# Kernel optimization log

Hardware: AMD Instinct MI355X
Metric: run time of the kernel (lower is better)

## Reference

```python
import jax, jax.numpy as jnp
import numpy as np

EPS = 1e-5

def _binarize(x):
    # torch.sign with 0 -> +1 (module maps sign==0 to 1)
    return jnp.where(x >= 0, 1.0, -1.0).astype(x.dtype)

def _conv(x, w, stride):
    return jax.lax.conv_general_dilated(
        x, w, window_strides=(stride, stride), padding=((1, 1), (1, 1)),
        dimension_numbers=('NCHW', 'OIHW', 'NCHW'))

def _bn(x, g, b, m, v):
    # eval-mode BatchNorm2d with running stats
    inv = g / jnp.sqrt(v + EPS)
    return x * inv[None, :, None, None] + (b - m * inv)[None, :, None, None]

def setup_inputs() -> dict:
    key = jax.random.key(0)
    ks = jax.random.split(key, 16)
    d = {
        'x': jax.random.normal(ks[0], (32, 3, 224, 224), jnp.float32),
        'conv1_w': jax.random.normal(ks[1], (32, 3, 3, 3), jnp.float32),
        'conv2_w': jax.random.normal(ks[2], (64, 32, 3, 3), jnp.float32),
        'conv3_w': jax.random.normal(ks[3], (128, 64, 3, 3), jnp.float32),
        'bn1_g': jax.random.normal(ks[4], (32,), jnp.float32),
        'bn1_b': jax.random.normal(ks[5], (32,), jnp.float32),
        'bn1_m': jax.random.normal(ks[6], (32,), jnp.float32),
        'bn1_v': jax.random.uniform(ks[7], (32,), jnp.float32, 0.5, 1.5),
        'bn2_g': jax.random.normal(ks[8], (64,), jnp.float32),
        'bn2_b': jax.random.normal(ks[9], (64,), jnp.float32),
        'bn2_m': jax.random.normal(ks[10], (64,), jnp.float32),
        'bn2_v': jax.random.uniform(ks[11], (64,), jnp.float32, 0.5, 1.5),
        'bn3_g': jax.random.normal(ks[12], (128,), jnp.float32),
        'bn3_b': jax.random.normal(ks[13], (128,), jnp.float32),
        'bn3_m': jax.random.normal(ks[14], (128,), jnp.float32),
        'bn3_v': jax.random.uniform(ks[15], (128,), jnp.float32, 0.5, 1.5),
        'fc_w': jax.random.normal(jax.random.fold_in(key, 99), (2, 128), jnp.float32) * 0.1,
        'fc_b': jnp.zeros((2,), jnp.float32),
    }
    return d

def reference(x, conv1_w, conv2_w, conv3_w,
              bn1_g, bn1_b, bn1_m, bn1_v,
              bn2_g, bn2_b, bn2_m, bn2_v,
              bn3_g, bn3_b, bn3_m, bn3_v,
              fc_w, fc_b):
    # layer 1: binarized conv -> BN -> sign
    h = _binarize(_bn(_conv(_binarize(x), _binarize(conv1_w), 1), bn1_g, bn1_b, bn1_m, bn1_v))  # [B,32,224,224]
    # layer 2 (stride 2)
    h = _binarize(_bn(_conv(_binarize(h), _binarize(conv2_w), 2), bn2_g, bn2_b, bn2_m, bn2_v))  # [B,64,112,112]
    # layer 3 (stride 2)
    h = _binarize(_bn(_conv(_binarize(h), _binarize(conv3_w), 2), bn3_g, bn3_b, bn3_m, bn3_v))  # [B,128,56,56]
    # adaptive avg pool to 1x1 + fc
    h = jnp.mean(h, axis=(2, 3))  # [B,128]
    return h @ fc_w.T + fc_b      # [B,2]
```

## Files before the change

### kernel.cpp

```cpp
#include <hip/hip_runtime.h>
#include <cstdint>
#include <cstddef>


__device__ __align__(16) uint32_t g_h1p[32 * 224 * 224];
__device__ __align__(16) uint32_t g_h2lo[32 * 112 * 112];
__device__ __align__(16) uint32_t g_h2hi[32 * 112 * 112];
__device__ uint32_t g_w1p[32];
__device__ uint32_t g_w2p[576];
__device__ uint64_t g_w3p[1152];
__device__ float    g_inv1[32],  g_sh1[32];
__device__ float    g_inv2[64],  g_sh2[64];
__device__ float    g_inv3[128], g_sh3[128];
__device__ int      g_thr1[32];
__device__ uint32_t g_pol1;
__device__ int      g_thr2[64];
__device__ uint32_t g_pol2[2];
__device__ int      g_acc[32 * 128];

__device__ __forceinline__ int bn_neg(int s, float inv, float sh) {
    float y = __fadd_rn(__fmul_rn((float)s, inv), sh);
    return (y < 0.0f) ? 1 : 0;
}

__global__ void prep_kernel(
    const float* __restrict__ w1, const float* __restrict__ w2, const float* __restrict__ w3,
    const float* __restrict__ g1, const float* __restrict__ b1, const float* __restrict__ m1, const float* __restrict__ v1,
    const float* __restrict__ g2, const float* __restrict__ b2, const float* __restrict__ m2, const float* __restrict__ v2,
    const float* __restrict__ g3, const float* __restrict__ b3, const float* __restrict__ m3, const float* __restrict__ v3)
{
    int tid = blockIdx.x * blockDim.x + threadIdx.x;
    int lt  = threadIdx.x;

    if (tid < 32 * 128) g_acc[tid] = 0;

    if (tid < 32) {
        uint32_t m = 0;
        for (int t = 0; t < 27; ++t)
            m |= (w1[tid * 27 + t] < 0.0f ? 1u : 0u) << t;
        g_w1p[tid] = m;
    }
    if (tid < 576) {
        int oc = tid / 9, tap = tid % 9, ky = tap / 3, kx = tap % 3;
        uint32_t m = 0;
        for (int ic = 0; ic < 32; ++ic)
            m |= (w2[((oc * 32 + ic) * 3 + ky) * 3 + kx] < 0.0f ? 1u : 0u) << ic;
        g_w2p[tid] = m;
    }
    if (tid < 1152) {
        int oc = tid / 9, tap = tid % 9, ky = tap / 3, kx = tap % 3;
        uint64_t m = 0;
        for (int ic = 0; ic < 64; ++ic)
            m |= (uint64_t)(w3[((oc * 64 + ic) * 3 + ky) * 3 + kx] < 0.0f ? 1u : 0u) << ic;
        g_w3p[tid] = m;
    }

    if (blockIdx.x == 0) {
        if (lt < 32) {
            float inv = __fdiv_rn(g1[lt], __fsqrt_rn(__fadd_rn(v1[lt], 1e-5f)));
            g_inv1[lt] = inv;
            g_sh1[lt] = __fsub_rn(b1[lt], __fmul_rn(m1[lt], inv));
        } else if (lt < 96) {
            int c = lt - 32;
            float inv = __fdiv_rn(g2[c], __fsqrt_rn(__fadd_rn(v2[c], 1e-5f)));
            g_inv2[c] = inv;
            g_sh2[c] = __fsub_rn(b2[c], __fmul_rn(m2[c], inv));
        } else if (lt < 224) {
            int c = lt - 96;
            float inv = __fdiv_rn(g3[c], __fsqrt_rn(__fadd_rn(v3[c], 1e-5f)));
            g_inv3[c] = inv;
            g_sh3[c] = __fsub_rn(b3[c], __fmul_rn(m3[c], inv));
        }
        __syncthreads();

        __shared__ uint32_t p1bits[32];
        __shared__ uint32_t p2bits[64];
        if (lt < 32) {
            float inv = g_inv1[lt], sh = g_sh1[lt];
            int P = bn_neg(27 - 2 * 27, inv, sh);
            int M = 28;
            for (int m = 0; m <= 27; ++m)
                if (bn_neg(27 - 2 * m, inv, sh) == P) { M = m; break; }
            g_thr1[lt] = M;
            p1bits[lt] = (uint32_t)P;
        }
        if (lt >= 64 && lt < 128) {
            int c = lt - 64;
            float inv = g_inv2[c], sh = g_sh2[c];
            int P = bn_neg(288 - 2 * 288, inv, sh);
            int M = 289;
            for (int m = 0; m <= 288; ++m)
                if (bn_neg(288 - 2 * m, inv, sh) == P) { M = m; break; }
            g_thr2[c] = M;
            p2bits[c] = (uint32_t)P;
        }
        __syncthreads();
        if (lt == 0) {
            uint32_t p = 0;
            for (int i = 0; i < 32; ++i) p |= p1bits[i] << i;
            g_pol1 = p;
            uint32_t plo = 0, phi = 0;
            for (int i = 0; i < 32; ++i) { plo |= p2bits[i] << i; phi |= p2bits[32 + i] << i; }
            g_pol2[0] = plo; g_pol2[1] = phi;
        }
    }
}

__global__ void layer1_kernel(const float* __restrict__ x)
{
    int idx = blockIdx.x * blockDim.x + threadIdx.x;
    const int total = 32 * 224 * 56;
    if (idx >= total) return;
    int xq = idx % 56;
    int t  = idx / 56;
    int yy = t % 224;
    int b  = t / 224;
    int xx0 = xq * 4;

    const float* xb = x + (size_t)b * 3 * 224 * 224;
    uint32_t outw[4];

    bool interior = (yy >= 1) && (yy <= 222) && (xq >= 1) && (xq <= 54);
    if (interior) {
        uint32_t cb[3][3];
#pragma unroll
        for (int ic = 0; ic < 3; ++ic)
#pragma unroll
        for (int r = 0; r < 3; ++r) {
            const float* p = xb + ((size_t)ic * 224 + (yy - 1 + r)) * 224 + (xx0 - 1);
            uint32_t bits = 0;
#pragma unroll
            for (int j = 0; j < 6; ++j)
                bits |= (p[j] < 0.0f ? 1u : 0u) << j;
            cb[ic][r] = bits;
        }
        uint32_t xm[4];
#pragma unroll
        for (int p = 0; p < 4; ++p) {
            uint32_t m = 0;
#pragma unroll
            for (int ic = 0; ic < 3; ++ic)
#pragma unroll
            for (int r = 0; r < 3; ++r)
                m |= ((cb[ic][r] >> p) & 7u) << (ic * 9 + r * 3);
            xm[p] = m;
        }
#pragma unroll
        for (int p = 0; p < 4; ++p) outw[p] = 0;
#pragma unroll
        for (int oc = 0; oc < 32; ++oc) {
            uint32_t w = g_w1p[oc];
            int M = g_thr1[oc];
#pragma unroll
            for (int p = 0; p < 4; ++p) {
                int mm = __popc(xm[p] ^ w);
                outw[p] |= (mm < M ? 1u : 0u) << oc;
            }
        }
        uint32_t pol = g_pol1;
#pragma unroll
        for (int p = 0; p < 4; ++p) outw[p] ^= pol;
    } else {
#pragma unroll
        for (int p = 0; p < 4; ++p) {
            int xx = xx0 + p;
            uint32_t xmask = 0, vmask = 0;
#pragma unroll
            for (int ky = 0; ky < 3; ++ky) {
                int iy = yy - 1 + ky;
                bool vy = (iy >= 0 && iy < 224);
#pragma unroll
                for (int kx = 0; kx < 3; ++kx) {
                    int ix = xx - 1 + kx;
                    bool v = vy && (ix >= 0) && (ix < 224);
                    if (v) {
                        int sp = ky * 3 + kx;
#pragma unroll
                        for (int ic = 0; ic < 3; ++ic) {
                            float val = xb[((size_t)ic * 224 + iy) * 224 + ix];
                            xmask |= (val < 0.0f ? 1u : 0u) << (ic * 9 + sp);
                            vmask |= 1u << (ic * 9 + sp);
                        }
                    }
                }
            }
            int nvalid = __popc(vmask);
            uint32_t ow = 0;
#pragma unroll
            for (int oc = 0; oc < 32; ++oc) {
                int mism = __popc((xmask ^ g_w1p[oc]) & vmask);
                int s = nvalid - 2 * mism;
                float y = __fadd_rn(__fmul_rn((float)s, g_inv1[oc]), g_sh1[oc]);
                ow |= (y < 0.0f ? 1u : 0u) << oc;
            }
            outw[p] = ow;
        }
    }
    uint4 o = make_uint4(outw[0], outw[1], outw[2], outw[3]);
    *(uint4*)&g_h1p[((size_t)b * 224 + yy) * 224 + xx0] = o;
}

__global__ void layer2_kernel()
{
    int half = blockIdx.y;
    int idx = blockIdx.x * blockDim.x + threadIdx.x;
    const int total = 32 * 112 * 112;
    if (idx >= total) return;
    int ox = idx % 112;
    int t = idx / 112;
    int oy = t % 112;
    int b = t / 112;

    const uint32_t* hb = g_h1p + (size_t)b * 224 * 224;
    const uint32_t* wp = g_w2p + half * 288;
    uint32_t outw = 0;

    if (ox >= 1 && oy >= 1) {
        uint32_t hw[9];
#pragma unroll
        for (int ky = 0; ky < 3; ++ky) {
            const uint32_t* row = hb + (2 * oy - 1 + ky) * 224 + (2 * ox - 1);
            hw[ky * 3 + 0] = row[0];
            hw[ky * 3 + 1] = row[1];
            hw[ky * 3 + 2] = row[2];
        }
        const int* thr = g_thr2 + half * 32;
        for (int oc = 0; oc < 32; ++oc) {
            int m = 0;
#pragma unroll
            for (int tt = 0; tt < 9; ++tt)
                m += __popc(hw[tt] ^ wp[oc * 9 + tt]);
            outw |= (m < thr[oc] ? 1u : 0u) << oc;
        }
        outw ^= g_pol2[half];
    } else {
        uint32_t hw[9];
        bool tv[9];
        int nvt = 0;
#pragma unroll
        for (int ky = 0; ky < 3; ++ky) {
            int iy = 2 * oy - 1 + ky;
            bool vy = (iy >= 0 && iy < 224);
#pragma unroll
            for (int kx = 0; kx < 3; ++kx) {
                int ix = 2 * ox - 1 + kx;
                bool v = vy && (ix >= 0) && (ix < 224);
                int tt = ky * 3 + kx;
                tv[tt] = v;
                nvt += v ? 1 : 0;
                hw[tt] = v ? hb[iy * 224 + ix] : 0u;
            }
        }
        int base = 32 * nvt;
        const float* invp = g_inv2 + half * 32;
        const float* shp  = g_sh2  + half * 32;
        for (int oc = 0; oc < 32; ++oc) {
            int s = 0;
#pragma unroll
            for (int tt = 0; tt < 9; ++tt) {
                uint32_t w = wp[oc * 9 + tt];
                s += __popc(hw[tt] ^ (tv[tt] ? w : 0u));
            }
            int val = base - 2 * s;
            float y = __fadd_rn(__fmul_rn((float)val, invp[oc]), shp[oc]);
            outw |= (y < 0.0f ? 1u : 0u) << oc;
        }
    }
    if (half == 0) g_h2lo[idx] = outw; else g_h2hi[idx] = outw;
}

__global__ void layer3_kernel()
{
    int ocq = blockIdx.z;
    int b = blockIdx.y;
    int pix = blockIdx.x * blockDim.x + threadIdx.x;
    bool valid = pix < 56 * 56;
    int oy = valid ? pix / 56 : 0;
    int ox = valid ? pix % 56 : 0;

    const uint32_t* hlo = g_h2lo + (size_t)b * 112 * 112;
    const uint32_t* hhi = g_h2hi + (size_t)b * 112 * 112;
    uint64_t hw[9];
    bool tv[9];
    int nvt = 0;
#pragma unroll
    for (int ky = 0; ky < 3; ++ky) {
        int iy = 2 * oy - 1 + ky;
        bool vy = (iy >= 0 && iy < 112);
#pragma unroll
        for (int kx = 0; kx < 3; ++kx) {
            int ix = 2 * ox - 1 + kx;
            bool v = valid && vy && (ix >= 0) && (ix < 112);
            int tt = ky * 3 + kx;
            tv[tt] = v;
            nvt += v ? 1 : 0;
            hw[tt] = v ? ((uint64_t)hlo[iy * 112 + ix] | ((uint64_t)hhi[iy * 112 + ix] << 32)) : 0ull;
        }
    }
    int base = 64 * nvt;
    int lane = threadIdx.x & 63;
    unsigned long long am = __ballot(valid ? 1 : 0);
    int nact = __popcll(am);

    const uint64_t* wp = g_w3p + ocq * 288;
    const float* invp = g_inv3 + ocq * 32;
    const float* shp  = g_sh3  + ocq * 32;
    for (int oc = 0; oc < 32; ++oc) {
        int s = 0;
#pragma unroll
        for (int tt = 0; tt < 9; ++tt) {
            uint64_t w = wp[oc * 9 + tt];
            s += __popcll(hw[tt] ^ (tv[tt] ? w : 0ull));
        }
        int val = base - 2 * s;
        float y = __fadd_rn(__fmul_rn((float)val, invp[oc]), shp[oc]);
        int neg = (valid && y < 0.0f) ? 1 : 0;
        unsigned long long bm = __ballot(neg);
        if (lane == 0) {
            int cneg = __popcll(bm);
            atomicAdd(&g_acc[b * 128 + ocq * 32 + oc], nact - 2 * cneg);
        }
    }
}

__global__ void fc_kernel(
    const float* __restrict__ fc_w, const float* __restrict__ fc_b,
    float* __restrict__ out)
{
    int tid = threadIdx.x;
    if (tid >= 64) return;
    int b = tid >> 1, k = tid & 1;
    float s = fc_b[k];
    for (int oc = 0; oc < 128; ++oc) {
        float h = __fdiv_rn((float)g_acc[b * 128 + oc], 3136.0f);
        s = __fadd_rn(s, __fmul_rn(h, fc_w[k * 128 + oc]));
    }
    out[b * 2 + k] = s;
}

extern "C" void kernel_launch(void* const* d_in, const int* in_sizes, int n_in,
                              void* d_out, int out_size, void* d_ws, size_t ws_size,
                              hipStream_t stream)
{
    const float* x   = (const float*)d_in[0];
    const float* w1  = (const float*)d_in[1];
    const float* w2  = (const float*)d_in[2];
    const float* w3  = (const float*)d_in[3];
    const float* g1  = (const float*)d_in[4];
    const float* b1  = (const float*)d_in[5];
    const float* m1  = (const float*)d_in[6];
    const float* v1  = (const float*)d_in[7];
    const float* g2  = (const float*)d_in[8];
    const float* b2  = (const float*)d_in[9];
    const float* m2  = (const float*)d_in[10];
    const float* v2  = (const float*)d_in[11];
    const float* g3  = (const float*)d_in[12];
    const float* b3  = (const float*)d_in[13];
    const float* m3  = (const float*)d_in[14];
    const float* v3  = (const float*)d_in[15];
    const float* fcw = (const float*)d_in[16];
    const float* fcb = (const float*)d_in[17];
    float* out = (float*)d_out;
    (void)d_ws; (void)ws_size; (void)in_sizes; (void)n_in; (void)out_size;

    prep_kernel<<<16, 256, 0, stream>>>(w1, w2, w3,
        g1, b1, m1, v1, g2, b2, m2, v2, g3, b3, m3, v3);

    {
        int total = 32 * 224 * 56;
        layer1_kernel<<<(total + 255) / 256, 256, 0, stream>>>(x);
    }
    {
        int total = 32 * 112 * 112;
        dim3 grid((total + 255) / 256, 2);
        layer2_kernel<<<grid, 256, 0, stream>>>();
    }
    {
        dim3 grid((56 * 56 + 255) / 256, 32, 4);
        layer3_kernel<<<grid, 256, 0, stream>>>();
    }
    fc_kernel<<<1, 64, 0, stream>>>(fcw, fcb, out);
}
```

Measured before the change: 233.7 us.

## Split interior and border work into separate blocks with per-pattern padding thresholds

Layers 1 and 2 now give interior pixels and border pixels their own block ranges, so warps no longer diverge between the fast popcount path and the slow float BN path. For each border pattern the prep kernel precomputes a threshold that folds in the invalid padded taps, so border pixels can use a plain popcount compare as well. Layer 1's interior loads switch to float4 reads. In exchange the prep kernel does more serial work in block 0, including threshold searches for three tap-count classes, and the border index mapping is more involved.

```diff
diff --git a/kernel.cpp b/kernel.cpp
--- a/kernel.cpp
+++ b/kernel.cpp
@@ -12,10 +12,10 @@
 __device__ float    g_inv1[32],  g_sh1[32];
 __device__ float    g_inv2[64],  g_sh2[64];
 __device__ float    g_inv3[128], g_sh3[128];
-__device__ int      g_thr1[32];
-__device__ uint32_t g_pol1;
-__device__ int      g_thr2[64];
-__device__ uint32_t g_pol2[2];
+__device__ int      g_Mb1[9 * 32];
+__device__ uint32_t g_pol1pk[9];
+__device__ int      g_Mb2[4 * 64];
+__device__ uint32_t g_pol2pk[4 * 2];
 __device__ int      g_acc[32 * 128];
 
 __device__ __forceinline__ int bn_neg(int s, float inv, float sh) {
@@ -34,19 +34,6 @@
 
     if (tid < 32 * 128) g_acc[tid] = 0;
 
-    if (tid < 32) {
-        uint32_t m = 0;
-        for (int t = 0; t < 27; ++t)
-            m |= (w1[tid * 27 + t] < 0.0f ? 1u : 0u) << t;
-        g_w1p[tid] = m;
-    }
-    if (tid < 576) {
-        int oc = tid / 9, tap = tid % 9, ky = tap / 3, kx = tap % 3;
-        uint32_t m = 0;
-        for (int ic = 0; ic < 32; ++ic)
-            m |= (w2[((oc * 32 + ic) * 3 + ky) * 3 + kx] < 0.0f ? 1u : 0u) << ic;
-        g_w2p[tid] = m;
-    }
     if (tid < 1152) {
         int oc = tid / 9, tap = tid % 9, ky = tap / 3, kx = tap % 3;
         uint64_t m = 0;
@@ -55,83 +42,138 @@
         g_w3p[tid] = m;
     }
 
-    if (blockIdx.x == 0) {
-        if (lt < 32) {
-            float inv = __fdiv_rn(g1[lt], __fsqrt_rn(__fadd_rn(v1[lt], 1e-5f)));
-            g_inv1[lt] = inv;
-            g_sh1[lt] = __fsub_rn(b1[lt], __fmul_rn(m1[lt], inv));
-        } else if (lt < 96) {
-            int c = lt - 32;
-            float inv = __fdiv_rn(g2[c], __fsqrt_rn(__fadd_rn(v2[c], 1e-5f)));
-            g_inv2[c] = inv;
-            g_sh2[c] = __fsub_rn(b2[c], __fmul_rn(m2[c], inv));
-        } else if (lt < 224) {
-            int c = lt - 96;
-            float inv = __fdiv_rn(g3[c], __fsqrt_rn(__fadd_rn(v3[c], 1e-5f)));
-            g_inv3[c] = inv;
-            g_sh3[c] = __fsub_rn(b3[c], __fmul_rn(m3[c], inv));
-        }
-        __syncthreads();
-
-        __shared__ uint32_t p1bits[32];
-        __shared__ uint32_t p2bits[64];
-        if (lt < 32) {
-            float inv = g_inv1[lt], sh = g_sh1[lt];
-            int P = bn_neg(27 - 2 * 27, inv, sh);
-            int M = 28;
-            for (int m = 0; m <= 27; ++m)
-                if (bn_neg(27 - 2 * m, inv, sh) == P) { M = m; break; }
-            g_thr1[lt] = M;
-            p1bits[lt] = (uint32_t)P;
-        }
-        if (lt >= 64 && lt < 128) {
-            int c = lt - 64;
-            float inv = g_inv2[c], sh = g_sh2[c];
-            int P = bn_neg(288 - 2 * 288, inv, sh);
-            int M = 289;
-            for (int m = 0; m <= 288; ++m)
-                if (bn_neg(288 - 2 * m, inv, sh) == P) { M = m; break; }
-            g_thr2[c] = M;
-            p2bits[c] = (uint32_t)P;
-        }
-        __syncthreads();
-        if (lt == 0) {
+    if (blockIdx.x != 0) return;
+    for (int i = lt; i < 32; i += 256) {
+        uint32_t m = 0;
+        for (int t = 0; t < 27; ++t)
+            m |= (w1[i * 27 + t] < 0.0f ? 1u : 0u) << t;
+        g_w1p[i] = m;
+    }
+    for (int i = lt; i < 576; i += 256) {
+        int oc = i / 9, tap = i % 9, ky = tap / 3, kx = tap % 3;
+        uint32_t m = 0;
+        for (int ic = 0; ic < 32; ++ic)
+            m |= (w2[((oc * 32 + ic) * 3 + ky) * 3 + kx] < 0.0f ? 1u : 0u) << ic;
+        g_w2p[i] = m;
+    }
+    if (lt < 32) {
+        float inv = __fdiv_rn(g1[lt], __fsqrt_rn(__fadd_rn(v1[lt], 1e-5f)));
+        g_inv1[lt] = inv;
+        g_sh1[lt] = __fsub_rn(b1[lt], __fmul_rn(m1[lt], inv));
+    } else if (lt < 96) {
+        int c = lt - 32;
+        float inv = __fdiv_rn(g2[c], __fsqrt_rn(__fadd_rn(v2[c], 1e-5f)));
+        g_inv2[c] = inv;
+        g_sh2[c] = __fsub_rn(b2[c], __fmul_rn(m2[c], inv));
+    } else if (lt < 224) {
+        int c = lt - 96;
+        float inv = __fdiv_rn(g3[c], __fsqrt_rn(__fadd_rn(v3[c], 1e-5f)));
+        g_inv3[c] = inv;
+        g_sh3[c] = __fsub_rn(b3[c], __fmul_rn(m3[c], inv));
+    }
+    __syncthreads();
+
+    __shared__ int sM1[3][32], sP1[3][32];
+    __shared__ int sM2[3][64], sP2[3][64];
+    if (lt < 32) {
+        int oc = lt;
+        float inv = g_inv1[oc], sh = g_sh1[oc];
+        const int nvs[3] = {12, 18, 27};
+        for (int k = 0; k < 3; ++k) {
+            int nv = nvs[k];
+            int P = bn_neg(-nv, inv, sh);
+            int M = nv + 1;
+            for (int m = 0; m <= nv; ++m)
+                if (bn_neg(nv - 2 * m, inv, sh) == P) { M = m; break; }
+            sM1[k][oc] = M; sP1[k][oc] = P;
+        }
+    } else if (lt >= 64 && lt < 128) {
+        int oc = lt - 64;
+        float inv = g_inv2[oc], sh = g_sh2[oc];
+        const int nvs[3] = {128, 192, 288};
+        for (int k = 0; k < 3; ++k) {
+            int nv = nvs[k];
+            int P = bn_neg(-nv, inv, sh);
+            int M = nv + 1;
+            for (int m = 0; m <= nv; ++m)
+                if (bn_neg(nv - 2 * m, inv, sh) == P) { M = m; break; }
+            sM2[k][oc] = M; sP2[k][oc] = P;
+        }
+    }
+    __syncthreads();
+
+    if (lt < 288) {
+        int pat = lt / 32, oc = lt % 32;
+        int py = pat / 3, px = pat % 3;
+        uint32_t invm = 0;
+        for (int ic = 0; ic < 3; ++ic)
+            for (int r = 0; r < 3; ++r)
+                for (int c = 0; c < 3; ++c) {
+                    bool inval = (py == 0 && r == 0) || (py == 2 && r == 2) ||
+                                 (px == 0 && c == 0) || (px == 2 && c == 2);
+                    if (inval) invm |= 1u << (ic * 9 + r * 3 + c);
+                }
+        int nv = 3 * (3 - (py != 1 ? 1 : 0)) * (3 - (px != 1 ? 1 : 0));
+        int cls = (nv == 27) ? 2 : ((nv == 18) ? 1 : 0);
+        g_Mb1[pat * 32 + oc] = sM1[cls][oc] + __popc(g_w1p[oc] & invm);
+    }
+    {
+        int pat = lt / 64, oc = lt % 64;
+        uint32_t tm = (pat == 0) ? 0u : (pat == 1 ? 0x07u : (pat == 2 ? 0x49u : 0x4Fu));
+        int cls = (pat == 0) ? 2 : (pat == 3 ? 0 : 1);
+        int corr = 0;
+        for (int tt = 0; tt < 9; ++tt)
+            if ((tm >> tt) & 1) corr += __popc(g_w2p[oc * 9 + tt]);
+        g_Mb2[pat * 64 + oc] = sM2[cls][oc] + corr;
+    }
+    if (lt == 0) {
+        for (int pat = 0; pat < 9; ++pat) {
+            int py = pat / 3, px = pat % 3;
+            int nv = 3 * (3 - (py != 1 ? 1 : 0)) * (3 - (px != 1 ? 1 : 0));
+            int cls = (nv == 27) ? 2 : ((nv == 18) ? 1 : 0);
             uint32_t p = 0;
-            for (int i = 0; i < 32; ++i) p |= p1bits[i] << i;
-            g_pol1 = p;
+            for (int i = 0; i < 32; ++i) p |= (uint32_t)sP1[cls][i] << i;
+            g_pol1pk[pat] = p;
+        }
+        for (int pat = 0; pat < 4; ++pat) {
+            int cls = (pat == 0) ? 2 : (pat == 3 ? 0 : 1);
             uint32_t plo = 0, phi = 0;
-            for (int i = 0; i < 32; ++i) { plo |= p2bits[i] << i; phi |= p2bits[32 + i] << i; }
-            g_pol2[0] = plo; g_pol2[1] = phi;
-        }
-    }
-}
-
+            for (int i = 0; i < 32; ++i) {
+                plo |= (uint32_t)sP2[cls][i] << i;
+                phi |= (uint32_t)sP2[cls][32 + i] << i;
+            }
+            g_pol2pk[pat * 2 + 0] = plo;
+            g_pol2pk[pat * 2 + 1] = phi;
+        }
+    }
+}
+
+#define L1_NBI 1499
 __global__ void layer1_kernel(const float* __restrict__ x)
 {
-    int idx = blockIdx.x * blockDim.x + threadIdx.x;
-    const int total = 32 * 224 * 56;
-    if (idx >= total) return;
-    int xq = idx % 56;
-    int t  = idx / 56;
-    int yy = t % 224;
-    int b  = t / 224;
-    int xx0 = xq * 4;
-
-    const float* xb = x + (size_t)b * 3 * 224 * 224;
-    uint32_t outw[4];
-
-    bool interior = (yy >= 1) && (yy <= 222) && (xq >= 1) && (xq <= 54);
-    if (interior) {
+    if (blockIdx.x < L1_NBI) {
+        int idx = blockIdx.x * 256 + threadIdx.x;
+        if (idx >= 32 * 222 * 54) return;
+        int t = idx;
+        int xq = 1 + t % 54; t /= 54;
+        int yy = 1 + t % 222;
+        int b  = t / 222;
+        int xx0 = xq * 4;
+
+        const float* xb = x + (size_t)b * 3 * 224 * 224;
         uint32_t cb[3][3];
 #pragma unroll
         for (int ic = 0; ic < 3; ++ic)
 #pragma unroll
         for (int r = 0; r < 3; ++r) {
-            const float* p = xb + ((size_t)ic * 224 + (yy - 1 + r)) * 224 + (xx0 - 1);
-            uint32_t bits = 0;
-#pragma unroll
-            for (int j = 0; j < 6; ++j)
-                bits |= (p[j] < 0.0f ? 1u : 0u) << j;
+            const float4* f = (const float4*)(xb + ((size_t)ic * 224 + (yy - 1 + r)) * 224 + (xx0 - 4));
+            float4 a = f[0], m = f[1], c = f[2];
+            uint32_t bits =  (a.w < 0.0f ? 1u : 0u)
+                          | ((m.x < 0.0f ? 1u : 0u) << 1)
+                          | ((m.y < 0.0f ? 1u : 0u) << 2)
+                          | ((m.z < 0.0f ? 1u : 0u) << 3)
+                          | ((m.w < 0.0f ? 1u : 0u) << 4)
+                          | ((c.x < 0.0f ? 1u : 0u) << 5);
             cb[ic][r] = bits;
         }
         uint32_t xm[4];
@@ -145,77 +187,74 @@
                 m |= ((cb[ic][r] >> p) & 7u) << (ic * 9 + r * 3);
             xm[p] = m;
         }
-#pragma unroll
-        for (int p = 0; p < 4; ++p) outw[p] = 0;
+        uint32_t outw[4] = {0, 0, 0, 0};
 #pragma unroll
         for (int oc = 0; oc < 32; ++oc) {
             uint32_t w = g_w1p[oc];
-            int M = g_thr1[oc];
+            int M = g_Mb1[4 * 32 + oc];
 #pragma unroll
             for (int p = 0; p < 4; ++p) {
                 int mm = __popc(xm[p] ^ w);
                 outw[p] |= (mm < M ? 1u : 0u) << oc;
             }
         }
-        uint32_t pol = g_pol1;
-#pragma unroll
-        for (int p = 0; p < 4; ++p) outw[p] ^= pol;
+        uint32_t pol = g_pol1pk[4];
+        uint4 o = make_uint4(outw[0] ^ pol, outw[1] ^ pol, outw[2] ^ pol, outw[3] ^ pol);
+        *(uint4*)&g_h1p[((size_t)b * 224 + yy) * 224 + xx0] = o;
     } else {
-#pragma unroll
-        for (int p = 0; p < 4; ++p) {
-            int xx = xx0 + p;
-            uint32_t xmask = 0, vmask = 0;
-#pragma unroll
-            for (int ky = 0; ky < 3; ++ky) {
-                int iy = yy - 1 + ky;
-                bool vy = (iy >= 0 && iy < 224);
-#pragma unroll
-                for (int kx = 0; kx < 3; ++kx) {
-                    int ix = xx - 1 + kx;
-                    bool v = vy && (ix >= 0) && (ix < 224);
-                    if (v) {
-                        int sp = ky * 3 + kx;
-#pragma unroll
-                        for (int ic = 0; ic < 3; ++ic) {
-                            float val = xb[((size_t)ic * 224 + iy) * 224 + ix];
-                            xmask |= (val < 0.0f ? 1u : 0u) << (ic * 9 + sp);
-                            vmask |= 1u << (ic * 9 + sp);
-                        }
-                    }
+        int i = (blockIdx.x - L1_NBI) * 256 + threadIdx.x;
+        int b = i / 2224;
+        int r = i % 2224;
+        int yy, xx;
+        if (r < 448) { yy = (r < 224) ? 0 : 223; xx = r % 224; }
+        else { int r2 = r - 448; yy = 1 + (r2 >> 3); int k = r2 & 7; xx = (k < 4) ? k : (216 + k); }
+
+        const float* xb = x + (size_t)b * 3 * 224 * 224;
+        uint32_t xmask = 0;
+#pragma unroll
+        for (int ky = 0; ky < 3; ++ky) {
+            int iy = yy - 1 + ky;
+            if (iy < 0 || iy > 223) continue;
+#pragma unroll
+            for (int kx = 0; kx < 3; ++kx) {
+                int ix = xx - 1 + kx;
+                if (ix < 0 || ix > 223) continue;
+                int sp = ky * 3 + kx;
+#pragma unroll
+                for (int ic = 0; ic < 3; ++ic) {
+                    float v = xb[((size_t)ic * 224 + iy) * 224 + ix];
+                    xmask |= (v < 0.0f ? 1u : 0u) << (ic * 9 + sp);
                 }
             }
-            int nvalid = __popc(vmask);
-            uint32_t ow = 0;
-#pragma unroll
-            for (int oc = 0; oc < 32; ++oc) {
-                int mism = __popc((xmask ^ g_w1p[oc]) & vmask);
-                int s = nvalid - 2 * mism;
-                float y = __fadd_rn(__fmul_rn((float)s, g_inv1[oc]), g_sh1[oc]);
-                ow |= (y < 0.0f ? 1u : 0u) << oc;
-            }
-            outw[p] = ow;
-        }
-    }
-    uint4 o = make_uint4(outw[0], outw[1], outw[2], outw[3]);
-    *(uint4*)&g_h1p[((size_t)b * 224 + yy) * 224 + xx0] = o;
-}
-
+        }
+        int py = (yy == 0) ? 0 : ((yy == 223) ? 2 : 1);
+        int px = (xx == 0) ? 0 : ((xx == 223) ? 2 : 1);
+        int pat = py * 3 + px;
+        uint32_t ow = 0;
+        for (int oc = 0; oc < 32; ++oc) {
+            uint32_t w = g_w1p[oc];
+            int mm = __popc(xmask ^ w);
+            int thr = g_Mb1[pat * 32 + oc];
+            ow |= (mm < thr ? 1u : 0u) << oc;
+        }
+        ow ^= g_pol1pk[pat];
+        g_h1p[((size_t)b * 224 + yy) * 224 + xx] = ow;
+    }
+}
+
+#define L2_NBI 3081
 __global__ void layer2_kernel()
 {
-    int half = blockIdx.y;
-    int idx = blockIdx.x * blockDim.x + threadIdx.x;
-    const int total = 32 * 112 * 112;
-    if (idx >= total) return;
-    int ox = idx % 112;
-    int t = idx / 112;
-    int oy = t % 112;
-    int b = t / 112;
-
-    const uint32_t* hb = g_h1p + (size_t)b * 224 * 224;
-    const uint32_t* wp = g_w2p + half * 288;
-    uint32_t outw = 0;
-
-    if (ox >= 1 && oy >= 1) {
+    if (blockIdx.x < L2_NBI) {
+        int idx = blockIdx.x * 256 + threadIdx.x;
+        if (idx >= 32 * 2 * 111 * 111) return;
+        int t = idx;
+        int ox = 1 + t % 111; t /= 111;
+        int oy = 1 + t % 111; t /= 111;
+        int half = t & 1;
+        int b = t >> 1;
+
+        const uint32_t* hb = g_h1p + (size_t)b * 224 * 224;
         uint32_t hw[9];
 #pragma unroll
         for (int ky = 0; ky < 3; ++ky) {
@@ -224,49 +263,55 @@
             hw[ky * 3 + 1] = row[1];
             hw[ky * 3 + 2] = row[2];
         }
-        const int* thr = g_thr2 + half * 32;
+        const uint32_t* wp = g_w2p + half * 288;
+        const int* thr = g_Mb2 + half * 32;
+        uint32_t ow = 0;
         for (int oc = 0; oc < 32; ++oc) {
-            int m = 0;
+            int mm = 0;
 #pragma unroll
             for (int tt = 0; tt < 9; ++tt)
-                m += __popc(hw[tt] ^ wp[oc * 9 + tt]);
-            outw |= (m < thr[oc] ? 1u : 0u) << oc;
-        }
-        outw ^= g_pol2[half];
+                mm += __popc(hw[tt] ^ wp[oc * 9 + tt]);
+            ow |= (mm < thr[oc] ? 1u : 0u) << oc;
+        }
+        ow ^= g_pol2pk[half];
+        uint32_t* dst = half ? g_h2hi : g_h2lo;
+        dst[((size_t)b * 112 + oy) * 112 + ox] = ow;
     } else {
+        int j = (blockIdx.x - L2_NBI) * 256 + threadIdx.x;
+        if (j >= 64 * 223) return;
+        int bh = j / 223;
+        int r  = j % 223;
+        int oy, ox;
+        if (r < 112) { oy = 0; ox = r; } else { ox = 0; oy = r - 111; }
+        int half = bh & 1, b = bh >> 1;
+
+        const uint32_t* hb = g_h1p + (size_t)b * 224 * 224;
         uint32_t hw[9];
-        bool tv[9];
-        int nvt = 0;
 #pragma unroll
         for (int ky = 0; ky < 3; ++ky) {
             int iy = 2 * oy - 1 + ky;
-            bool vy = (iy >= 0 && iy < 224);
 #pragma unroll
             for (int kx = 0; kx < 3; ++kx) {
                 int ix = 2 * ox - 1 + kx;
-                bool v = vy && (ix >= 0) && (ix < 224);
-                int tt = ky * 3 + kx;
-                tv[tt] = v;
-                nvt += v ? 1 : 0;
-                hw[tt] = v ? hb[iy * 224 + ix] : 0u;
+                bool v = (iy >= 0) && (ix >= 0);
+                hw[ky * 3 + kx] = v ? hb[iy * 224 + ix] : 0u;
             }
         }
-        int base = 32 * nvt;
-        const float* invp = g_inv2 + half * 32;
-        const float* shp  = g_sh2  + half * 32;
+        int pat = (oy == 0 ? 1 : 0) + (ox == 0 ? 2 : 0);
+        const uint32_t* wp = g_w2p + half * 288;
+        const int* thr = g_Mb2 + pat * 64 + half * 32;
+        uint32_t ow = 0;
         for (int oc = 0; oc < 32; ++oc) {
-            int s = 0;
-#pragma unroll
-            for (int tt = 0; tt < 9; ++tt) {
-                uint32_t w = wp[oc * 9 + tt];
-                s += __popc(hw[tt] ^ (tv[tt] ? w : 0u));
-            }
-            int val = base - 2 * s;
-            float y = __fadd_rn(__fmul_rn((float)val, invp[oc]), shp[oc]);
-            outw |= (y < 0.0f ? 1u : 0u) << oc;
-        }
-    }
-    if (half == 0) g_h2lo[idx] = outw; else g_h2hi[idx] = outw;
+            int mm = 0;
+#pragma unroll
+            for (int tt = 0; tt < 9; ++tt)
+                mm += __popc(hw[tt] ^ wp[oc * 9 + tt]);
+            ow |= (mm < thr[oc] ? 1u : 0u) << oc;
+        }
+        ow ^= g_pol2pk[pat * 2 + half];
+        uint32_t* dst = half ? g_h2hi : g_h2lo;
+        dst[((size_t)b * 112 + oy) * 112 + ox] = ow;
+    }
 }
 
 __global__ void layer3_kernel()
@@ -367,13 +412,10 @@
         g1, b1, m1, v1, g2, b2, m2, v2, g3, b3, m3, v3);
 
     {
-        int total = 32 * 224 * 56;
-        layer1_kernel<<<(total + 255) / 256, 256, 0, stream>>>(x);
+        layer1_kernel<<<L1_NBI + 278, 256, 0, stream>>>(x);
     }
     {
-        int total = 32 * 112 * 112;
-        dim3 grid((total + 255) / 256, 2);
-        layer2_kernel<<<grid, 256, 0, stream>>>();
+        layer2_kernel<<<L2_NBI + 56, 256, 0, stream>>>();
     }
     {
         dim3 grid((56 * 56 + 255) / 256, 32, 4);
```

Result: faster. 222.0 us (-5.0%).
